# Optimization experiments

Hardware: AMD Instinct MI355X
Metric: run time of the kernel (lower is better)

## Reference

```python
import jax, jax.numpy as jnp
import numpy as np

B, S, D_IN, D_H = 4, 2048, 1024, 1024

def setup_inputs() -> dict:
    key = jax.random.key(0)
    kx, kq, kk, kv = jax.random.split(key, 4)
    # nn.Linear default init: U(-1/sqrt(fan_in), 1/sqrt(fan_in)); stored as [out, in]
    bound = 1.0 / np.sqrt(D_IN)
    x = jax.random.normal(kx, (B, S, D_IN), dtype=jnp.float32)
    W_q = jax.random.uniform(kq, (D_H, D_IN), jnp.float32, -bound, bound)
    W_k = jax.random.uniform(kk, (D_H, D_IN), jnp.float32, -bound, bound)
    W_v = jax.random.uniform(kv, (D_H, D_IN), jnp.float32, -bound, bound)
    return {"x": x, "W_q": W_q, "W_k": W_k, "W_v": W_v}

def reference(x, W_q, W_k, W_v):
    # Q = x @ W_q.T, etc. (nn.Linear with bias=False)
    Q = jnp.einsum('bsd,hd->bsh', x, W_q)
    K = jnp.einsum('bsd,hd->bsh', x, W_k)
    V = jnp.einsum('bsd,hd->bsh', x, W_v)
    # NOTE: original scales by sqrt(Q.shape[1]) == sqrt(seq_len), not sqrt(d)
    scale = 1.0 / jnp.sqrt(jnp.asarray(Q.shape[1], Q.dtype))
    scores = jnp.einsum('bqh,bkh->bqk', Q, K) * scale  # [B,S,S]
    attn = jax.nn.softmax(scores, axis=-1)
    return jnp.einsum('bqk,bkh->bqh', attn, V)
```

## Files before the change

kernel.cpp:

```cpp
#include <hip/hip_runtime.h>

typedef unsigned short ushort_t;
typedef __attribute__((ext_vector_type(8))) __bf16 bf16x8;
typedef __attribute__((ext_vector_type(4))) float floatx4;

__device__ __forceinline__ ushort_t f2bf(float f) {
    unsigned int u = __builtin_bit_cast(unsigned int, f);
    u = (u + 0x7fffu + ((u >> 16) & 1u)) >> 16;
    return (ushort_t)u;
}

__device__ __forceinline__ void async16(const ushort_t* g, ushort_t* l) {
    __builtin_amdgcn_global_load_lds(
        (const __attribute__((address_space(1))) unsigned int*)g,
        (__attribute__((address_space(3))) unsigned int*)l,
        16 , 0 , 0 );
}

__device__ __forceinline__ int sw(int row, int cg) {
    return ((row << 2) + ((cg ^ row ^ (row >> 2)) & 3)) << 3;
}

__device__ __forceinline__ int xcd_swz(int bid, int cpx) {
    return (bid & 7) * cpx + (bid >> 3);
}

template <int N>
__device__ __forceinline__ void vwait() {
    if constexpr (N == 0)      asm volatile("s_waitcnt vmcnt(0)" ::: "memory");
    else if constexpr (N == 3) asm volatile("s_waitcnt vmcnt(3)" ::: "memory");
    else if constexpr (N == 4) asm volatile("s_waitcnt vmcnt(4)" ::: "memory");
    else if constexpr (N == 6) asm volatile("s_waitcnt vmcnt(6)" ::: "memory");
    else if constexpr (N == 8) asm volatile("s_waitcnt vmcnt(8)" ::: "memory");
    else static_assert(N == 0, "unsupported vmcnt");
}

template <int BM, int BN, int IM, int IN, int NW, int NS>
__device__ __forceinline__ void gemm_core_p(
    const ushort_t* __restrict__ A, int lda,
    const ushort_t* __restrict__ B, int ldb,
    int K, int tile_m, int tile_n,
    ushort_t* buf,
    floatx4 (&acc)[IM][IN]) {

    constexpr int NT = NW * 64;
    constexpr int SA = BM * 4 / NT;
    constexpr int SB = BN * 4 / NT;
    constexpr int Q  = SA + SB;
    constexpr int SLOT = (BM + BN) * 32;
    constexpr int BOFF = BM * 32;

    const int tid  = threadIdx.x;
    const int lane = tid & 63;
    const int wave = tid >> 6;
    const int wm   = wave >> 1, wn = wave & 1;
    const int quad = lane >> 4;
    const int l16  = lane & 15;

#pragma unroll
    for (int i = 0; i < IM; i++)
#pragma unroll
        for (int j = 0; j < IN; j++) acc[i][j] = (floatx4){0.f, 0.f, 0.f, 0.f};

    const ushort_t* ga[SA];
    int la[SA];
#pragma unroll
    for (int s = 0; s < SA; s++) {
        int seg = tid + s * NT;
        int r = seg >> 2, c = (seg ^ r ^ (r >> 2)) & 3;
        ga[s] = A + (long)(r + tile_m) * lda + c * 8;
        la[s] = seg * 8;
    }
    const ushort_t* gb[SB];
    int lb[SB];
#pragma unroll
    for (int s = 0; s < SB; s++) {
        int seg = tid + s * NT;
        int r = seg >> 2, c = (seg ^ r ^ (r >> 2)) & 3;
        gb[s] = B + (long)(r + tile_n) * ldb + c * 8;
        lb[s] = BOFF + seg * 8;
    }

    const int nk = K >> 5;

#pragma unroll
    for (int p = 0; p < NS - 1; ++p) {
#pragma unroll
        for (int s = 0; s < SA; s++) async16(ga[s] + p * 32, buf + p * SLOT + la[s]);
#pragma unroll
        for (int s = 0; s < SB; s++) async16(gb[s] + p * 32, buf + p * SLOT + lb[s]);
    }

    int slot = 0, slot2 = NS - 1;
    for (int k = 0; k < nk; ++k) {
        const int rem = nk - 1 - k;
        if (rem >= NS - 2) {
            vwait<(NS - 2) * Q>();
        } else if (NS >= 4 && rem == 1) {
            vwait<Q>();
        } else {
            vwait<0>();
        }
        __builtin_amdgcn_s_barrier();
        asm volatile("" ::: "memory");

        if (k + NS - 1 < nk) {
            const int koff = (k + NS - 1) << 5;
            ushort_t* dst = buf + slot2 * SLOT;
#pragma unroll
            for (int s = 0; s < SA; s++) async16(ga[s] + koff, dst + la[s]);
#pragma unroll
            for (int s = 0; s < SB; s++) async16(gb[s] + koff, dst + lb[s]);
        }

        const ushort_t* as = buf + slot * SLOT;
        const ushort_t* bs = as + BOFF;
        bf16x8 af[IM], bfr[IN];
#pragma unroll
        for (int im = 0; im < IM; im++)
            af[im] = *(const bf16x8*)&as[sw(wm * IM * 16 + im * 16 + l16, quad)];
#pragma unroll
        for (int in = 0; in < IN; in++)
            bfr[in] = *(const bf16x8*)&bs[sw(wn * IN * 16 + in * 16 + l16, quad)];
#pragma unroll
        for (int im = 0; im < IM; im++)
#pragma unroll
            for (int in = 0; in < IN; in++)
                acc[im][in] = __builtin_amdgcn_mfma_f32_16x16x32_bf16(
                    af[im], bfr[in], acc[im][in], 0, 0, 0);

        slot  = (slot == NS - 1) ? 0 : slot + 1;
        slot2 = (slot2 == NS - 1) ? 0 : slot2 + 1;
    }
}

__global__ void prep_kernel(const float* __restrict__ x,
                            const float* __restrict__ wq,
                            const float* __restrict__ wk,
                            const float* __restrict__ wv,
                            ushort_t* __restrict__ xb,
                            ushort_t* __restrict__ wvb,
                            ushort_t* __restrict__ wqT,
                            ushort_t* __restrict__ wkT,
                            float* __restrict__ lsum) {
    const int bx = blockIdx.x;
    const int t = threadIdx.x;
    if (bx < 9216) {
        const float* src;
        ushort_t* dst;
        long g;
        if (bx < 8192) { src = x;  dst = xb;  g = ((long)bx * 256 + t) * 4; }
        else           { src = wv; dst = wvb; g = ((long)(bx - 8192) * 256 + t) * 4; }
        float4 v = *(const float4*)(src + g);
        ushort4 o;
        o.x = f2bf(v.x); o.y = f2bf(v.y); o.z = f2bf(v.z); o.w = f2bf(v.w);
        *(ushort4*)(dst + g) = o;
        return;
    }
    if (bx < 9224) {
        int idx = (bx - 9216) * 256 + t;
        ((float4*)lsum)[idx] = (float4){0.f, 0.f, 0.f, 0.f};
        return;
    }
    const int tt = bx - 9224;
    const float* src = (tt >= 256) ? wk : wq;
    ushort_t* dst = (tt >= 256) ? wkT : wqT;
    const int id = tt & 255;
    const int h0 = (id >> 4) * 64, d0 = (id & 15) * 64;
    __shared__ ushort_t tile[64 * 80];
    {
        int i = t >> 2, cg = (t & 3) << 4;
        const float4* p = (const float4*)(src + (long)(h0 + i) * 1024 + d0 + cg);
#pragma unroll
        for (int k = 0; k < 4; k++) {
            float4 v = p[k];
            ushort_t* q = &tile[i * 80 + cg + k * 4];
            q[0] = f2bf(v.x); q[1] = f2bf(v.y); q[2] = f2bf(v.z); q[3] = f2bf(v.w);
        }
    }
    __syncthreads();
    {
        int j = t >> 2, ig = (t & 3) << 4;
        ushort_t tmp[16];
#pragma unroll
        for (int k = 0; k < 16; k++) tmp[k] = tile[(ig + k) * 80 + j];
        ushort_t* o = dst + (long)(d0 + j) * 1024 + h0 + ig;
        *(uint4*)o = ((uint4*)tmp)[0];
        *(uint4*)(o + 8) = ((uint4*)tmp)[1];
    }
}

__global__ __launch_bounds__(512, 4) void gv_kernel(
    const ushort_t* __restrict__ wkT, const ushort_t* __restrict__ wqT,
    const ushort_t* __restrict__ wvb, const ushort_t* __restrict__ xb,
    ushort_t* __restrict__ Gb, ushort_t* __restrict__ VTb) {

    __shared__ __align__(16) ushort_t buf[3 * 384 * 32];

    const ushort_t *A, *B;
    ushort_t* C;
    int ldc, tile_m, tile_n;
    if (blockIdx.x < 32) {
        A = wkT; B = wqT; C = Gb; ldc = 1024;
        tile_m = (blockIdx.x >> 3) * 256;
        tile_n = (blockIdx.x & 7) * 128;
    } else {
        int id = blockIdx.x - 32;
        A = wvb; B = xb; C = VTb; ldc = 8192;
        tile_m = (id >> 6) * 256;
        tile_n = (id & 63) * 128;
    }

    floatx4 acc[4][4];
    gemm_core_p<256, 128, 4, 4, 8, 3>(A, 1024, B, 1024, 1024, tile_m, tile_n, buf, acc);

    const int lane = threadIdx.x & 63, wave = threadIdx.x >> 6;
    const int wm = wave >> 1, wn = wave & 1, quad = lane >> 4, l16 = lane & 15;
#pragma unroll
    for (int im = 0; im < 4; im++)
#pragma unroll
        for (int r = 0; r < 4; r++) {
            int row = tile_m + wm * 64 + im * 16 + quad * 4 + r;
#pragma unroll
            for (int in = 0; in < 4; in++) {
                int col = tile_n + wn * 64 + in * 16 + l16;
                C[(long)row * ldc + col] = f2bf(acc[im][in][r]);
            }
        }
}

__global__ __launch_bounds__(256) void y_kernel(
    const ushort_t* __restrict__ xb,
    const ushort_t* __restrict__ Gb,
    ushort_t* __restrict__ Yb) {

    __shared__ __align__(16) ushort_t buf[4 * 256 * 32];
    const int lin = xcd_swz(blockIdx.x, 64);
    const int tile_n = (lin & 7) * 128;
    const int tile_m = (lin >> 3) * 128;

    floatx4 acc[4][4];
    gemm_core_p<128, 128, 4, 4, 4, 4>(xb, 1024, Gb, 1024, 1024, tile_m, tile_n, buf, acc);

    const int lane = threadIdx.x & 63, wave = threadIdx.x >> 6;
    const int wm = wave >> 1, wn = wave & 1, quad = lane >> 4, l16 = lane & 15;
#pragma unroll
    for (int im = 0; im < 4; im++)
#pragma unroll
        for (int r = 0; r < 4; r++) {
            int row = tile_m + wm * 64 + im * 16 + quad * 4 + r;
#pragma unroll
            for (int in = 0; in < 4; in++) {
                int col = tile_n + wn * 64 + in * 16 + l16;
                Yb[(long)row * 1024 + col] = f2bf(acc[im][in][r]);
            }
        }
}

__global__ __launch_bounds__(512, 4) void pexp_kernel(
    const ushort_t* __restrict__ Yb,
    const ushort_t* __restrict__ xb,
    ushort_t* __restrict__ Pb,
    float* __restrict__ lsum) {

    __shared__ __align__(16) ushort_t buf[3 * 384 * 32];

    const int lin = xcd_swz(blockIdx.x, 64);
    const int z = lin >> 7;
    const int tile_m = ((lin >> 4) & 7) * 256;
    const int tile_n = (lin & 15) * 128;

    const ushort_t* A = Yb + (long)z * 2097152;
    const ushort_t* B = xb + (long)z * 2097152;
    ushort_t* C = Pb + (long)z * 4194304;
    float* l = lsum + z * 2048;

    floatx4 acc[4][4];
    gemm_core_p<256, 128, 4, 4, 8, 3>(A, 1024, B, 1024, 1024, tile_m, tile_n, buf, acc);

    const float scale = 0.022097086912079608f;
    const int lane = threadIdx.x & 63, wave = threadIdx.x >> 6;
    const int wm = wave >> 1, wn = wave & 1, quad = lane >> 4, l16 = lane & 15;
#pragma unroll
    for (int im = 0; im < 4; im++)
#pragma unroll
        for (int r = 0; r < 4; r++) {
            int row = tile_m + wm * 64 + im * 16 + quad * 4 + r;
            float psum = 0.f;
#pragma unroll
            for (int in = 0; in < 4; in++) {
                int col = tile_n + wn * 64 + in * 16 + l16;
                float e = __expf(acc[im][in][r] * scale);
                C[(long)row * 2048 + col] = f2bf(e);
                psum += e;
            }
            psum += __shfl_xor(psum, 1, 64);
            psum += __shfl_xor(psum, 2, 64);
            psum += __shfl_xor(psum, 4, 64);
            psum += __shfl_xor(psum, 8, 64);
            if (l16 == 0) atomicAdd(&l[row], psum);
        }
}

__global__ __launch_bounds__(256) void out_kernel(
    const ushort_t* __restrict__ Pb,
    const ushort_t* __restrict__ VTb,
    float* __restrict__ out,
    const float* __restrict__ lsum) {

    __shared__ __align__(16) ushort_t buf[4 * 256 * 32];

    const int lin = xcd_swz(blockIdx.x, 64);
    const int z = lin >> 7;
    const int tile_m = ((lin >> 3) & 15) * 128;
    const int tile_n = (lin & 7) * 128;

    const ushort_t* A = Pb + (long)z * 4194304;
    const ushort_t* B = VTb + (long)z * 2048;
    float* C = out + (long)z * 2097152;
    const float* l = lsum + z * 2048;

    floatx4 acc[4][4];
    gemm_core_p<128, 128, 4, 4, 4, 4>(A, 2048, B, 8192, 2048, tile_m, tile_n, buf, acc);

    const int lane = threadIdx.x & 63, wave = threadIdx.x >> 6;
    const int wm = wave >> 1, wn = wave & 1, quad = lane >> 4, l16 = lane & 15;
#pragma unroll
    for (int im = 0; im < 4; im++)
#pragma unroll
        for (int r = 0; r < 4; r++) {
            int row = tile_m + wm * 64 + im * 16 + quad * 4 + r;
            float li = 1.0f / l[row];
#pragma unroll
            for (int in = 0; in < 4; in++) {
                int col = tile_n + wn * 64 + in * 16 + l16;
                C[(long)row * 1024 + col] = acc[im][in][r] * li;
            }
        }
}

extern "C" void kernel_launch(void* const* d_in, const int* in_sizes, int n_in,
                              void* d_out, int out_size, void* d_ws, size_t ws_size,
                              hipStream_t stream) {
    const float* x  = (const float*)d_in[0];
    const float* wq = (const float*)d_in[1];
    const float* wk = (const float*)d_in[2];
    const float* wv = (const float*)d_in[3];

    ushort_t* xb  = (ushort_t*)d_ws;
    ushort_t* wvb = xb  + 8388608;
    ushort_t* wqT = wvb + 1048576;
    ushort_t* wkT = wqT + 1048576;
    ushort_t* Gb  = wkT + 1048576;
    ushort_t* Yb  = Gb  + 1048576;
    ushort_t* VTb = Yb  + 8388608;
    ushort_t* Pb  = VTb + 8388608;
    float*    lsum = (float*)(Pb + 16777216);
    float*    out  = (float*)d_out;

    prep_kernel<<<9736, 256, 0, stream>>>(x, wq, wk, wv, xb, wvb, wqT, wkT, lsum);

    gv_kernel<<<288, 512, 0, stream>>>(wkT, wqT, wvb, xb, Gb, VTb);

    y_kernel<<<512, 256, 0, stream>>>(xb, Gb, Yb);

    pexp_kernel<<<512, 512, 0, stream>>>(Yb, xb, Pb, lsum);

    out_kernel<<<512, 256, 0, stream>>>(Pb, VTb, out, lsum);
}
```

Baseline: 229.2 us.

## Use 256x256 tiles with phased ping-pong GEMM schedule in pexp kernel

Replaces the pexp kernel's 256x128 three-stage GEMM core with a new 256x256 tile routine. Each K-step is split into four MFMA phases separated by barriers, with async global-to-LDS loads interleaved and s_setprio raising priority around the MFMA blocks. The goal is more arithmetic per byte loaded and better overlap of loads with matrix work. In exchange it uses 128 KB of LDS per block, holds more accumulators per thread, runs half as many blocks with lower occupancy, and adds many barriers.

```diff
diff --git a/kernel.cpp b/kernel.cpp
--- a/kernel.cpp
+++ b/kernel.cpp
@@ -132,6 +132,163 @@
         slot  = (slot == NS - 1) ? 0 : slot + 1;
         slot2 = (slot2 == NS - 1) ? 0 : slot2 + 1;
     }
+}
+
+__device__ __forceinline__ void gemm256_8ph(
+    const ushort_t* __restrict__ A, int lda,
+    const ushort_t* __restrict__ B, int ldb,
+    int K, int tile_m, int tile_n,
+    ushort_t* buf,
+    floatx4 (&acc)[8][4]) {
+
+    const int tid  = threadIdx.x;
+    const int lane = tid & 63;
+    const int wave = tid >> 6;
+    const int wm   = wave >> 2;
+    const int wn   = wave & 3;
+    const int quad = lane >> 4;
+    const int l16  = lane & 15;
+
+#pragma unroll
+    for (int i = 0; i < 8; i++)
+#pragma unroll
+        for (int j = 0; j < 4; j++) acc[i][j] = (floatx4){0.f, 0.f, 0.f, 0.f};
+
+    const int srow = tid >> 3;
+    const int scg  = (tid & 7) ^ (srow & 7);
+    const ushort_t* gA = A + (long)(tile_m + srow) * lda + scg * 8;
+    const ushort_t* gB = B + (long)(tile_n + srow) * ldb + scg * 8;
+    ushort_t* const ld = buf + tid * 8;
+
+#define STA_(p, h, t)                                                          \
+    do {                                                                       \
+        async16(gA + (long)((h)*128)      * lda + (t)*64,                      \
+                ld + (p)*32768 + (h)*8192);                                    \
+        async16(gA + (long)((h)*128 + 64) * lda + (t)*64,                      \
+                ld + (p)*32768 + (h)*8192 + 4096);                             \
+    } while (0)
+#define STB_(p, h, t)                                                          \
+    do {                                                                       \
+        async16(gB + (long)((h)*128)      * ldb + (t)*64,                      \
+                ld + (p)*32768 + 16384 + (h)*8192);                            \
+        async16(gB + (long)((h)*128 + 64) * ldb + (t)*64,                      \
+                ld + (p)*32768 + 16384 + (h)*8192 + 4096);                     \
+    } while (0)
+
+    const int rb0 = l16 * 64 + (((quad)     ^ (l16 & 7)) << 3);
+    const int rb1 = l16 * 64 + (((quad + 4) ^ (l16 & 7)) << 3);
+    const int abase = wm * 8192;
+    const int bbase = 16384 + (wn >> 1) * 8192 + (wn & 1) * 4096;
+
+    const int nt = K >> 6;
+
+    STA_(0, 0, 0); STB_(0, 0, 0); STB_(0, 1, 0); STA_(0, 1, 0);
+    STB_(1, 0, 1); STB_(1, 1, 1); STA_(1, 0, 1);
+    asm volatile("s_waitcnt vmcnt(6)" ::: "memory");
+    __builtin_amdgcn_s_barrier();
+    asm volatile("" ::: "memory");
+
+    bf16x8 aR[4][2], bKc[2][2], bCc[2][2];
+
+    for (int t = 0; t < nt; ++t) {
+        const int p  = t & 1;
+        const int pn = p ^ 1;
+        const ushort_t* sb = buf + p * 32768;
+
+        if (t + 1 < nt) STA_(pn, 1, t + 1);
+#pragma unroll
+        for (int fr = 0; fr < 4; fr++) {
+            aR[fr][0] = *(const bf16x8*)&sb[abase + fr * 1024 + rb0];
+            aR[fr][1] = *(const bf16x8*)&sb[abase + fr * 1024 + rb1];
+        }
+#pragma unroll
+        for (int fc = 0; fc < 2; fc++) {
+            bKc[fc][0] = *(const bf16x8*)&sb[bbase + fc * 1024 + rb0];
+            bKc[fc][1] = *(const bf16x8*)&sb[bbase + fc * 1024 + rb1];
+        }
+        asm volatile("" ::: "memory");
+        __builtin_amdgcn_s_barrier();
+        __builtin_amdgcn_s_setprio(1);
+#pragma unroll
+        for (int fr = 0; fr < 4; fr++)
+#pragma unroll
+            for (int fc = 0; fc < 2; fc++) {
+                acc[fr][fc] = __builtin_amdgcn_mfma_f32_16x16x32_bf16(
+                    aR[fr][0], bKc[fc][0], acc[fr][fc], 0, 0, 0);
+                acc[fr][fc] = __builtin_amdgcn_mfma_f32_16x16x32_bf16(
+                    aR[fr][1], bKc[fc][1], acc[fr][fc], 0, 0, 0);
+            }
+        __builtin_amdgcn_s_setprio(0);
+        asm volatile("" ::: "memory");
+        __builtin_amdgcn_s_barrier();
+        asm volatile("" ::: "memory");
+
+#pragma unroll
+        for (int fc = 0; fc < 2; fc++) {
+            bCc[fc][0] = *(const bf16x8*)&sb[bbase + (fc + 2) * 1024 + rb0];
+            bCc[fc][1] = *(const bf16x8*)&sb[bbase + (fc + 2) * 1024 + rb1];
+        }
+        asm volatile("" ::: "memory");
+        __builtin_amdgcn_s_barrier();
+        __builtin_amdgcn_s_setprio(1);
+#pragma unroll
+        for (int fr = 0; fr < 4; fr++)
+#pragma unroll
+            for (int fc = 0; fc < 2; fc++) {
+                acc[fr][fc + 2] = __builtin_amdgcn_mfma_f32_16x16x32_bf16(
+                    aR[fr][0], bCc[fc][0], acc[fr][fc + 2], 0, 0, 0);
+                acc[fr][fc + 2] = __builtin_amdgcn_mfma_f32_16x16x32_bf16(
+                    aR[fr][1], bCc[fc][1], acc[fr][fc + 2], 0, 0, 0);
+            }
+        __builtin_amdgcn_s_setprio(0);
+        asm volatile("" ::: "memory");
+        __builtin_amdgcn_s_barrier();
+        asm volatile("" ::: "memory");
+
+        if (t + 2 < nt) STB_(p, 0, t + 2);
+#pragma unroll
+        for (int fr = 0; fr < 4; fr++) {
+            aR[fr][0] = *(const bf16x8*)&sb[abase + (fr + 4) * 1024 + rb0];
+            aR[fr][1] = *(const bf16x8*)&sb[abase + (fr + 4) * 1024 + rb1];
+        }
+        asm volatile("" ::: "memory");
+        __builtin_amdgcn_s_barrier();
+        __builtin_amdgcn_s_setprio(1);
+#pragma unroll
+        for (int fr = 0; fr < 4; fr++)
+#pragma unroll
+            for (int fc = 0; fc < 2; fc++) {
+                acc[fr + 4][fc + 2] = __builtin_amdgcn_mfma_f32_16x16x32_bf16(
+                    aR[fr][0], bCc[fc][0], acc[fr + 4][fc + 2], 0, 0, 0);
+                acc[fr + 4][fc + 2] = __builtin_amdgcn_mfma_f32_16x16x32_bf16(
+                    aR[fr][1], bCc[fc][1], acc[fr + 4][fc + 2], 0, 0, 0);
+            }
+        __builtin_amdgcn_s_setprio(0);
+        asm volatile("" ::: "memory");
+        __builtin_amdgcn_s_barrier();
+        asm volatile("" ::: "memory");
+
+        if (t + 2 < nt) { STB_(p, 1, t + 2); STA_(p, 0, t + 2); }
+        asm volatile("" ::: "memory");
+        __builtin_amdgcn_s_barrier();
+        __builtin_amdgcn_s_setprio(1);
+#pragma unroll
+        for (int fr = 0; fr < 4; fr++)
+#pragma unroll
+            for (int fc = 0; fc < 2; fc++) {
+                acc[fr + 4][fc] = __builtin_amdgcn_mfma_f32_16x16x32_bf16(
+                    aR[fr][0], bKc[fc][0], acc[fr + 4][fc], 0, 0, 0);
+                acc[fr + 4][fc] = __builtin_amdgcn_mfma_f32_16x16x32_bf16(
+                    aR[fr][1], bKc[fc][1], acc[fr + 4][fc], 0, 0, 0);
+            }
+        __builtin_amdgcn_s_setprio(0);
+        if (t + 2 < nt) vwait<6>();
+        else            vwait<0>();
+        __builtin_amdgcn_s_barrier();
+        asm volatile("" ::: "memory");
+    }
+#undef STA_
+#undef STB_
 }
 
 __global__ void prep_kernel(const float* __restrict__ x,
@@ -257,40 +414,40 @@
         }
 }
 
-__global__ __launch_bounds__(512, 4) void pexp_kernel(
+__global__ __launch_bounds__(512, 2) void pexp_kernel(
     const ushort_t* __restrict__ Yb,
     const ushort_t* __restrict__ xb,
     ushort_t* __restrict__ Pb,
     float* __restrict__ lsum) {
 
-    __shared__ __align__(16) ushort_t buf[3 * 384 * 32];
-
-    const int lin = xcd_swz(blockIdx.x, 64);
-    const int z = lin >> 7;
-    const int tile_m = ((lin >> 4) & 7) * 256;
-    const int tile_n = (lin & 15) * 128;
+    __shared__ __align__(16) ushort_t buf[65536];
+
+    const int lin = xcd_swz(blockIdx.x, 32);
+    const int z = lin >> 6;
+    const int tile_m = ((lin >> 3) & 7) * 256;
+    const int tile_n = (lin & 7) * 256;
 
     const ushort_t* A = Yb + (long)z * 2097152;
     const ushort_t* B = xb + (long)z * 2097152;
     ushort_t* C = Pb + (long)z * 4194304;
     float* l = lsum + z * 2048;
 
-    floatx4 acc[4][4];
-    gemm_core_p<256, 128, 4, 4, 8, 3>(A, 1024, B, 1024, 1024, tile_m, tile_n, buf, acc);
+    floatx4 acc[8][4];
+    gemm256_8ph(A, 1024, B, 1024, 1024, tile_m, tile_n, buf, acc);
 
     const float scale = 0.022097086912079608f;
     const int lane = threadIdx.x & 63, wave = threadIdx.x >> 6;
-    const int wm = wave >> 1, wn = wave & 1, quad = lane >> 4, l16 = lane & 15;
-#pragma unroll
-    for (int im = 0; im < 4; im++)
-#pragma unroll
-        for (int r = 0; r < 4; r++) {
-            int row = tile_m + wm * 64 + im * 16 + quad * 4 + r;
+    const int wm = wave >> 2, wn = wave & 3, quad = lane >> 4, l16 = lane & 15;
+#pragma unroll
+    for (int fr = 0; fr < 8; fr++)
+#pragma unroll
+        for (int rr = 0; rr < 4; rr++) {
+            int row = tile_m + wm * 128 + fr * 16 + quad * 4 + rr;
             float psum = 0.f;
 #pragma unroll
-            for (int in = 0; in < 4; in++) {
-                int col = tile_n + wn * 64 + in * 16 + l16;
-                float e = __expf(acc[im][in][r] * scale);
+            for (int fc = 0; fc < 4; fc++) {
+                int col = tile_n + wn * 64 + fc * 16 + l16;
+                float e = __expf(acc[fr][fc][rr] * scale);
                 C[(long)row * 2048 + col] = f2bf(e);
                 psum += e;
             }
@@ -359,12 +516,8 @@
     float*    out  = (float*)d_out;
 
     prep_kernel<<<9736, 256, 0, stream>>>(x, wq, wk, wv, xb, wvb, wqT, wkT, lsum);
-
     gv_kernel<<<288, 512, 0, stream>>>(wkT, wqT, wvb, xb, Gb, VTb);
-
     y_kernel<<<512, 256, 0, stream>>>(xb, Gb, Yb);
-
-    pexp_kernel<<<512, 512, 0, stream>>>(Yb, xb, Pb, lsum);
-
+    pexp_kernel<<<256, 512, 0, stream>>>(Yb, xb, Pb, lsum);
     out_kernel<<<512, 256, 0, stream>>>(Pb, VTb, out, lsum);
 }
```

Measured after the change: 230.9 us. About the same (+0.7%).
